# Kernel optimization log

Hardware: AMD Instinct MI355X
Metric: run time of the kernel (lower is better)

The kernel has to match this reference:

```python
import jax, jax.numpy as jnp
import numpy as np
from jax import lax

# pywt db4 decomposition filters (hardcoded to avoid pywt dependency)
DB4_DEC_LO = np.array([-0.010597401784997278, 0.032883011666982945,
                       0.030841381835986965, -0.18703481171888114,
                       -0.02798376941698385, 0.6308807679295904,
                       0.7148465705525415, 0.23037781330885523], dtype=np.float32)
DB4_DEC_HI = np.array([-0.23037781330885523, 0.7148465705525415,
                       -0.6308807679295904, -0.02798376941698385,
                       0.18703481171888114, 0.030841381835986965,
                       -0.032883011666982945, -0.010597401784997278], dtype=np.float32)

B, T, C = 32, 16384, 64

def setup_inputs() -> dict:
    key = jax.random.key(0)
    x = jax.random.normal(key, (B, T, C), dtype=jnp.float32)
    return {"x": x,
            "dec_lo": jnp.asarray(DB4_DEC_LO),
            "dec_hi": jnp.asarray(DB4_DEC_HI)}

def _depthwise_conv1d(xp, filt, channels):
    # xp: [B, L, C]; filt: [K]; depthwise stride-2 valid cross-correlation
    k = jnp.broadcast_to(filt[:, None, None], (filt.shape[0], 1, channels))  # [K,1,C]
    return lax.conv_general_dilated(
        xp, k, window_strides=(2,), padding='VALID',
        dimension_numbers=('NWC', 'WIO', 'NWC'),
        feature_group_count=channels)

def reference(x, dec_lo, dec_hi):
    channels = x.shape[-1]
    filter_length = dec_lo.shape[0]          # 8 for db4
    pad = filter_length - 1                   # 7
    crop = pad // 2                           # 3
    xp = jnp.pad(x, ((0, 0), (pad, pad), (0, 0)), mode='reflect')
    approx = _depthwise_conv1d(xp, dec_lo, channels)[:, crop:-crop, :]
    detail = _depthwise_conv1d(xp, dec_hi, channels)[:, crop:-crop, :]
    # original concatenates all approx channels then all detail channels
    return jnp.concatenate([approx, detail], axis=-1)  # [B, T/2-2, 2C]
```

## Files before the change

kernel.cpp:

```cpp
#include <hip/hip_runtime.h>


#define BT   32
#define TT   16384
#define CC   64
#define T2   8190
#define OC   128
#define TPT  8

__global__ __launch_bounds__(256) void dwt_db4_kernel(
    const float* __restrict__ x,
    const float* __restrict__ dec_lo,
    const float* __restrict__ dec_hi,
    float* __restrict__ out)
{
    const int cg   = threadIdx.x;
    const int tw   = threadIdx.y;
    const int tile = blockIdx.x;
    const int b    = blockIdx.y;

    const int c4 = cg * 4;
    const int t0 = (tile * 16 + tw) * TPT;

    float flo[8], fhi[8];
    #pragma unroll
    for (int k = 0; k < 8; ++k) { flo[k] = dec_lo[k]; fhi[k] = dec_hi[k]; }

    const float* __restrict__ xb = x   + (size_t)b * TT * CC;
    float*       __restrict__ ob = out + (size_t)b * T2 * OC;

    const int m0 = 2 * t0 - 1;

    float4 w[8];
    #pragma unroll
    for (int i = 0; i < 6; ++i) {
        int m  = m0 + i;
        int mm = m < 0 ? -m : m;
        mm     = mm > (TT - 1) ? 2 * (TT - 1) - mm : mm;
        w[i] = *reinterpret_cast<const float4*>(xb + (size_t)mm * CC + c4);
    }

    #pragma unroll
    for (int j = 0; j < TPT; ++j) {
        {
            int m  = m0 + 2 * j + 6;
            int mm = m > (TT - 1) ? 2 * (TT - 1) - m : m;
            w[6] = *reinterpret_cast<const float4*>(xb + (size_t)mm * CC + c4);
            m  = m0 + 2 * j + 7;
            mm = m > (TT - 1) ? 2 * (TT - 1) - m : m;
            w[7] = *reinterpret_cast<const float4*>(xb + (size_t)mm * CC + c4);
        }

        const int t = t0 + j;
        if (t < T2) {
            float4 alo, ahi;
            alo.x = alo.y = alo.z = alo.w = 0.0f;
            ahi.x = ahi.y = ahi.z = ahi.w = 0.0f;
            #pragma unroll
            for (int k = 0; k < 8; ++k) {
                alo.x = fmaf(flo[k], w[k].x, alo.x);
                alo.y = fmaf(flo[k], w[k].y, alo.y);
                alo.z = fmaf(flo[k], w[k].z, alo.z);
                alo.w = fmaf(flo[k], w[k].w, alo.w);
                ahi.x = fmaf(fhi[k], w[k].x, ahi.x);
                ahi.y = fmaf(fhi[k], w[k].y, ahi.y);
                ahi.z = fmaf(fhi[k], w[k].z, ahi.z);
                ahi.w = fmaf(fhi[k], w[k].w, ahi.w);
            }
            *reinterpret_cast<float4*>(ob + (size_t)t * OC + c4)      = alo;
            *reinterpret_cast<float4*>(ob + (size_t)t * OC + CC + c4) = ahi;
        }

        #pragma unroll
        for (int i = 0; i < 6; ++i) w[i] = w[i + 2];
    }
}

extern "C" void kernel_launch(void* const* d_in, const int* in_sizes, int n_in,
                              void* d_out, int out_size, void* d_ws, size_t ws_size,
                              hipStream_t stream)
{
    const float* x      = (const float*)d_in[0];
    const float* dec_lo = (const float*)d_in[1];
    const float* dec_hi = (const float*)d_in[2];
    float*       out    = (float*)d_out;

    dim3 block(16, 16);
    dim3 grid((T2 + 16 * TPT - 1) / (16 * TPT), BT);

    hipLaunchKernelGGL(dwt_db4_kernel, grid, block, 0, stream,
                       x, dec_lo, dec_hi, out);
}
```

Baseline: 242.3 us.

## Preload full input window per thread, cut outputs per thread, use nontemporal stores

Each thread now produces 4 output rows instead of 8 and loads its whole 15-row input window up front, rather than streaming two rows per iteration. This exposes more independent loads in flight and gives a grid with more blocks. Outputs are written with nontemporal stores to avoid polluting the cache. The cost is more redundant input reads at the overlap between neighbouring windows and higher register use.

```diff
diff --git a/kernel.cpp b/kernel.cpp
--- a/kernel.cpp
+++ b/kernel.cpp
@@ -6,73 +6,69 @@
 #define CC   64
 #define T2   8190
 #define OC   128
-#define TPT  8
+#define QPT  4
+#define NQ   ((T2 + QPT - 1) / QPT)
 
-__global__ __launch_bounds__(256) void dwt_db4_kernel(
+typedef float vf4 __attribute__((ext_vector_type(4)));
+
+__global__ __launch_bounds__(256) void dwt_db4_quad_kernel(
     const float* __restrict__ x,
     const float* __restrict__ dec_lo,
     const float* __restrict__ dec_hi,
     float* __restrict__ out)
 {
-    const int cg   = threadIdx.x;
-    const int tw   = threadIdx.y;
-    const int tile = blockIdx.x;
+    const int tid  = threadIdx.x;
+    const int cg   = tid & 15;
+    const int qs   = tid >> 4;
+    const int quad = blockIdx.x * 16 + qs;
     const int b    = blockIdx.y;
+    if (quad >= NQ) return;
 
+    const int t0 = quad * QPT;
     const int c4 = cg * 4;
-    const int t0 = (tile * 16 + tw) * TPT;
 
     float flo[8], fhi[8];
     #pragma unroll
     for (int k = 0; k < 8; ++k) { flo[k] = dec_lo[k]; fhi[k] = dec_hi[k]; }
 
-    const float* __restrict__ xb = x   + (size_t)b * TT * CC;
-    float*       __restrict__ ob = out + (size_t)b * T2 * OC;
+    const float* __restrict__ xb = x + (size_t)b * TT * CC;
 
     const int m0 = 2 * t0 - 1;
-
-    float4 w[8];
+    vf4 w[15];
     #pragma unroll
-    for (int i = 0; i < 6; ++i) {
+    for (int i = 0; i < 15; ++i) {
         int m  = m0 + i;
         int mm = m < 0 ? -m : m;
         mm     = mm > (TT - 1) ? 2 * (TT - 1) - mm : mm;
-        w[i] = *reinterpret_cast<const float4*>(xb + (size_t)mm * CC + c4);
+        w[i] = *reinterpret_cast<const vf4*>(xb + (size_t)mm * CC + c4);
+    }
+
+    vf4 alo[QPT], ahi[QPT];
+    #pragma unroll
+    for (int j = 0; j < QPT; ++j) {
+        alo[j] = (vf4)0.0f;
+        ahi[j] = (vf4)0.0f;
     }
 
     #pragma unroll
-    for (int j = 0; j < TPT; ++j) {
-        {
-            int m  = m0 + 2 * j + 6;
-            int mm = m > (TT - 1) ? 2 * (TT - 1) - m : m;
-            w[6] = *reinterpret_cast<const float4*>(xb + (size_t)mm * CC + c4);
-            m  = m0 + 2 * j + 7;
-            mm = m > (TT - 1) ? 2 * (TT - 1) - m : m;
-            w[7] = *reinterpret_cast<const float4*>(xb + (size_t)mm * CC + c4);
+    for (int j = 0; j < QPT; ++j) {
+        #pragma unroll
+        for (int k = 0; k < 8; ++k) {
+            const vf4 v = w[2 * j + k];
+            alo[j] += flo[k] * v;
+            ahi[j] += fhi[k] * v;
         }
+    }
 
-        const int t = t0 + j;
-        if (t < T2) {
-            float4 alo, ahi;
-            alo.x = alo.y = alo.z = alo.w = 0.0f;
-            ahi.x = ahi.y = ahi.z = ahi.w = 0.0f;
-            #pragma unroll
-            for (int k = 0; k < 8; ++k) {
-                alo.x = fmaf(flo[k], w[k].x, alo.x);
-                alo.y = fmaf(flo[k], w[k].y, alo.y);
-                alo.z = fmaf(flo[k], w[k].z, alo.z);
-                alo.w = fmaf(flo[k], w[k].w, alo.w);
-                ahi.x = fmaf(fhi[k], w[k].x, ahi.x);
-                ahi.y = fmaf(fhi[k], w[k].y, ahi.y);
-                ahi.z = fmaf(fhi[k], w[k].z, ahi.z);
-                ahi.w = fmaf(fhi[k], w[k].w, ahi.w);
-            }
-            *reinterpret_cast<float4*>(ob + (size_t)t * OC + c4)      = alo;
-            *reinterpret_cast<float4*>(ob + (size_t)t * OC + CC + c4) = ahi;
+    float* __restrict__ ob = out + (size_t)b * T2 * OC + (size_t)t0 * OC;
+    #pragma unroll
+    for (int j = 0; j < QPT; ++j) {
+        if (t0 + j < T2) {
+            __builtin_nontemporal_store(alo[j],
+                reinterpret_cast<vf4*>(ob + (size_t)j * OC + c4));
+            __builtin_nontemporal_store(ahi[j],
+                reinterpret_cast<vf4*>(ob + (size_t)j * OC + CC + c4));
         }
-
-        #pragma unroll
-        for (int i = 0; i < 6; ++i) w[i] = w[i + 2];
     }
 }
 
@@ -85,9 +81,9 @@
     const float* dec_hi = (const float*)d_in[2];
     float*       out    = (float*)d_out;
 
-    dim3 block(16, 16);
-    dim3 grid((T2 + 16 * TPT - 1) / (16 * TPT), BT);
+    dim3 block(256);
+    dim3 grid((NQ + 15) / 16, BT);
 
-    hipLaunchKernelGGL(dwt_db4_kernel, grid, block, 0, stream,
+    hipLaunchKernelGGL(dwt_db4_quad_kernel, grid, block, 0, stream,
                        x, dec_lo, dec_hi, out);
 }
```

Measured after the change: 230.6 us. 4.8% less time.
